# Performance work log

Measured on AMD Instinct MI355X. Metric: run time of the kernel, lower is better.

Reference implementation:

```python
import jax, jax.numpy as jnp
import numpy as np

D_MODEL, D_STATE, D_CONV, EXPAND, N_HEADS = 1024, 64, 4, 2, 8
D_INNER = EXPAND * D_MODEL
D_HEAD = D_INNER // N_HEADS
B, T = 2, 2048
EPS = 1e-6


def setup_inputs() -> dict:
    key = jax.random.key(0)
    ks = jax.random.split(key, 12)
    s = 0.02
    return {
        "x": jax.random.normal(ks[0], (B, T, D_MODEL), jnp.float32),
        "norm_w": jnp.ones((D_MODEL,), jnp.float32),
        "in_w": jax.random.normal(ks[1], (2 * D_INNER, D_MODEL), jnp.float32) * s,
        "conv_w": jax.random.normal(ks[2], (D_INNER, 1, D_CONV), jnp.float32) * s,
        "conv_b": jnp.zeros((D_INNER,), jnp.float32),
        "A_log": jax.random.normal(ks[3], (N_HEADS,), jnp.float32),
        "B_w": jax.random.normal(ks[4], (N_HEADS * D_STATE, D_INNER), jnp.float32) * s,
        "C_w": jax.random.normal(ks[5], (N_HEADS * D_STATE, D_INNER), jnp.float32) * s,
        "dt_w": jax.random.normal(ks[6], (N_HEADS, D_INNER), jnp.float32) * s,
        "dt_b": jnp.zeros((N_HEADS,), jnp.float32),
        "D": jnp.ones((N_HEADS,), jnp.float32),
        "out_w": jax.random.normal(ks[7], (D_MODEL, D_INNER), jnp.float32) * s,
    }


def _rmsnorm(x, w):
    var = jnp.mean(jnp.square(x), axis=-1, keepdims=True)
    return x * jax.lax.rsqrt(var + EPS) * w


def _silu(x):
    return x * jax.nn.sigmoid(x)


def reference(x, norm_w, in_w, conv_w, conv_b, A_log, B_w, C_w, dt_w, dt_b, D, out_w):
    residual = x
    xn = _rmsnorm(x, norm_w)
    xz = xn @ in_w.T                                   # (B,T,2*D_INNER)
    x_ssm, z = jnp.split(xz, 2, axis=-1)

    # causal depthwise conv1d (torch pads both sides by K-1 then slices [:T] == left pad only)
    xc = jnp.transpose(x_ssm, (0, 2, 1))               # (B,C,T)
    xc = jax.lax.conv_general_dilated(
        xc, conv_w, window_strides=(1,), padding=[(D_CONV - 1, 0)],
        feature_group_count=D_INNER,
        dimension_numbers=("NCH", "OIH", "NCH"))
    xc = xc + conv_b[None, :, None]
    x_ssm = _silu(jnp.transpose(xc, (0, 2, 1)))        # (B,T,D_INNER)

    dt = jax.nn.softplus(x_ssm @ dt_w.T + dt_b)        # (B,T,H)
    Bm = (x_ssm @ B_w.T).reshape(B, T, N_HEADS, D_STATE)
    Cm = (x_ssm @ C_w.T).reshape(B, T, N_HEADS, D_STATE)
    xh = x_ssm.reshape(B, T, N_HEADS, D_HEAD)
    A = -jnp.exp(A_log)                                # (H,)

    # time-major for scan
    dt_t = jnp.transpose(dt, (1, 0, 2))                # (T,B,H)
    B_t = jnp.transpose(Bm, (1, 0, 2, 3))              # (T,B,H,N)
    C_t = jnp.transpose(Cm, (1, 0, 2, 3))
    x_t = jnp.transpose(xh, (1, 0, 2, 3))              # (T,B,H,D)

    def step(h, inp):
        dtt, bt, ct, xt = inp
        dA = jnp.exp(dtt * A)[..., None, None]         # (B,H,1,1)
        h = dA * h + dtt[..., None, None] * bt[..., :, None] * xt[..., None, :]
        y = jnp.einsum("bhn,bhnd->bhd", ct, h)
        return h, y

    h0 = jnp.zeros((B, N_HEADS, D_STATE, D_HEAD), x.dtype)
    _, ys = jax.lax.scan(step, h0, (dt_t, B_t, C_t, x_t))  # ys: (T,B,H,D)
    y = jnp.transpose(ys, (1, 0, 2, 3))                # (B,T,H,D)
    y = y + xh * D[None, None, :, None]
    y = y.reshape(B, T, D_INNER)
    y = y * _silu(z)
    out = y @ out_w.T
    return residual + out
```

## Files before the change

kernel.cpp:

```cpp
#include <hip/hip_runtime.h>
#include <hip/hip_bf16.h>
#include <math.h>

#define D_MODEL 1024
#define D_STATE 64
#define D_CONV  4
#define D_INNER 2048
#define N_HEADS 8
#define D_HEAD  256
#define BATCH   2
#define SEQ     2048
#define ROWS    (BATCH*SEQ)
#define NCHUNK  32
#define BCN     1152
#define EPS     1e-6f

typedef __attribute__((ext_vector_type(2))) unsigned short ushort2v;
typedef __attribute__((ext_vector_type(4))) unsigned short ushort4v;
typedef __attribute__((ext_vector_type(8))) unsigned short ushort8v;
typedef __attribute__((ext_vector_type(8))) short short8v;
typedef __attribute__((ext_vector_type(4))) float f32x4;

__device__ __forceinline__ float silu_f(float x){ return x / (1.0f + __expf(-x)); }
__device__ __forceinline__ float softplus_f(float x){ return (x > 20.0f) ? x : log1pf(__expf(x)); }
__device__ __forceinline__ float bf2f(unsigned short u){
    union { unsigned int i; float f; } v; v.i = ((unsigned int)u) << 16; return v.f;
}
__device__ __forceinline__ unsigned short f2bf_bits(float f){
    __hip_bfloat16 h = __float2bfloat16(f);
    return *(unsigned short*)&h;
}
__device__ __forceinline__ void gload_lds16(const void* g, void* l){
    __builtin_amdgcn_global_load_lds((const __attribute__((address_space(1))) void*)g,
                                     (__attribute__((address_space(3))) void*)l, 16, 0, 0);
}
__device__ __forceinline__ void vmw(int n){
    switch(n){
        case 0:  asm volatile("s_waitcnt vmcnt(0)"  ::: "memory"); break;
        case 2:  asm volatile("s_waitcnt vmcnt(2)"  ::: "memory"); break;
        case 3:  asm volatile("s_waitcnt vmcnt(3)"  ::: "memory"); break;
        case 4:  asm volatile("s_waitcnt vmcnt(4)"  ::: "memory"); break;
        case 6:  asm volatile("s_waitcnt vmcnt(6)"  ::: "memory"); break;
        default: asm volatile("s_waitcnt vmcnt(0)"  ::: "memory"); break;
    }
}

__global__ __launch_bounds__(256) void prep_kernel(const float* __restrict__ in_w,
                                                   const float* __restrict__ out_w,
                                                   const float* __restrict__ B_w,
                                                   const float* __restrict__ C_w,
                                                   const float* __restrict__ dt_w,
                                                   unsigned short* __restrict__ inw_bf,
                                                   unsigned short* __restrict__ outw_bf,
                                                   unsigned short* __restrict__ BCw_bf){
    int i = blockIdx.x * 256 + threadIdx.x;
    const float* src; unsigned short* dst; int j;
    if (i < 1048576)      { src = in_w;  dst = inw_bf;            j = i; }
    else if (i < 1572864) { src = out_w; dst = outw_bf;           j = i - 1048576; }
    else if (i < 1835008) { src = B_w;   dst = BCw_bf;            j = i - 1572864; }
    else if (i < 2097152) { src = C_w;   dst = BCw_bf + 1048576;  j = i - 1835008; }
    else {
        int k = i - 2097152;
        int drow = k >> 9;
        int col4 = k & 511;
        ushort4v o = {0,0,0,0};
        if (drow < 8){
            float4 v = ((const float4*)(dt_w + (size_t)drow*D_INNER))[col4];
            o[0] = f2bf_bits(v.x); o[1] = f2bf_bits(v.y);
            o[2] = f2bf_bits(v.z); o[3] = f2bf_bits(v.w);
        }
        ((ushort4v*)(BCw_bf + (size_t)(1024 + drow)*D_INNER))[col4] = o;
        return;
    }
    float4 v = ((const float4*)src)[j];
    ushort4v o;
    o[0] = f2bf_bits(v.x); o[1] = f2bf_bits(v.y);
    o[2] = f2bf_bits(v.z); o[3] = f2bf_bits(v.w);
    ((ushort4v*)dst)[j] = o;
}

__global__ __launch_bounds__(256) void rmsnorm_kernel(const float* __restrict__ x,
                                                      const float* __restrict__ w,
                                                      unsigned short* __restrict__ xn){
    int row = blockIdx.x;
    int tid = threadIdx.x;
    const float4* xr = (const float4*)(x + (size_t)row * D_MODEL);
    float4 a = xr[tid];
    float ss = a.x*a.x + a.y*a.y + a.z*a.z + a.w*a.w;
    #pragma unroll
    for (int i = 1; i < 64; i <<= 1) ss += __shfl_xor(ss, i);
    __shared__ float red[4];
    int lane = tid & 63, wid = tid >> 6;
    if (lane == 0) red[wid] = ss;
    __syncthreads();
    float tot = red[0] + red[1] + red[2] + red[3];
    float scale = rsqrtf(tot * (1.0f / D_MODEL) + EPS);
    float4 wv = ((const float4*)w)[tid];
    ushort4v o;
    o[0] = f2bf_bits(a.x * scale * wv.x);
    o[1] = f2bf_bits(a.y * scale * wv.y);
    o[2] = f2bf_bits(a.z * scale * wv.z);
    o[3] = f2bf_bits(a.w * scale * wv.w);
    ((ushort4v*)(xn + (size_t)row * D_MODEL))[tid] = o;
}

__global__ __launch_bounds__(512) void gemm_in512(const unsigned short* __restrict__ A,
                                                  const unsigned short* __restrict__ W,
                                                  unsigned short* __restrict__ Cout0,
                                                  unsigned short* __restrict__ Cout1){
    const int K = D_MODEL;
    __shared__ unsigned short As[2][256*32];
    __shared__ unsigned short Bs[2][128*32];
    int tid = threadIdx.x;
    int bid = blockIdx.x;
    int x = bid & 7;
    int r = bid >> 3;
    int m0 = ((x & 3)*4 + (r >> 4)) * 256;
    int n0 = ((x >> 2)*16 + (r & 15)) * 128;

    int lane = tid & 63;
    int w = tid >> 6;
    int wrow = w >> 1, wcol = w & 1;
    f32x4 acc[4][4];
    #pragma unroll
    for (int i = 0; i < 4; ++i)
        #pragma unroll
        for (int j = 0; j < 4; ++j) acc[i][j] = (f32x4){0.f,0.f,0.f,0.f};

    int g0 = tid >> 3, s0 = tid & 7;
    int swz0 = (s0*16) ^ ((g0&7)<<4);
    int r0 = 2*g0 + (swz0 >> 6);
    int c0e = (swz0 & 63) >> 1;
    const unsigned short* aS0 = A + (size_t)(m0 + r0)*K + c0e;
    const unsigned short* aS1 = aS0 + (size_t)128*K;
    const unsigned short* bS0 = W + (size_t)(n0 + r0)*K + c0e;

    int frow = lane & 15;
    int fkb  = (lane >> 4) * 16;
    int offA[4], offB[4];
    #pragma unroll
    for (int m = 0; m < 4; ++m){
        int rr = wrow*64 + m*16 + frow;
        int lb = (rr&1)*64 + fkb;
        offA[m] = (rr>>1)*128 + (lb ^ (((rr>>1)&7)<<4));
    }
    #pragma unroll
    for (int n = 0; n < 4; ++n){
        int rr = wcol*64 + n*16 + frow;
        int lb = (rr&1)*64 + fkb;
        offB[n] = (rr>>1)*128 + (lb ^ (((rr>>1)&7)<<4));
    }

    #define STAGE(buf, k0) do{ \
        gload_lds16(aS0 + (k0), &As[buf][(size_t)tid*8]); \
        gload_lds16(aS1 + (k0), &As[buf][(size_t)(tid+512)*8]); \
        gload_lds16(bS0 + (k0), &Bs[buf][(size_t)tid*8]); \
    }while(0)

    #define COMPUTE(buf, tt) do{ \
        short8v af[4], bf[4]; \
        _Pragma("unroll") \
        for (int m = 0; m < 4; ++m) af[m] = *(const short8v*)((const char*)As[buf] + offA[m]); \
        _Pragma("unroll") \
        for (int n = 0; n < 4; ++n) bf[n] = *(const short8v*)((const char*)Bs[buf] + offB[n]); \
        asm volatile("s_waitcnt lgkmcnt(0)" ::: "memory"); \
        __builtin_amdgcn_sched_barrier(0); \
        __builtin_amdgcn_s_barrier(); \
        if ((tt) + 2 < NT) STAGE(buf, (size_t)((tt)+2)*32); \
        _Pragma("unroll") \
        for (int m = 0; m < 4; ++m) \
            _Pragma("unroll") \
            for (int n = 0; n < 4; ++n) \
                acc[m][n] = __builtin_amdgcn_mfma_f32_16x16x32_bf16(af[m], bf[n], acc[m][n], 0, 0, 0); \
    }while(0)

    int NT = K >> 5;
    STAGE(0, 0);
    STAGE(1, 32);
    int t = 0;
    for (; t < NT-1; ++t){
        vmw(3);
        __builtin_amdgcn_sched_barrier(0);
        __builtin_amdgcn_s_barrier();
        COMPUTE(t & 1, t);
    }
    {
        vmw(0);
        __builtin_amdgcn_sched_barrier(0);
        __builtin_amdgcn_s_barrier();
        COMPUTE(t & 1, t);
    }
    #undef COMPUTE
    #undef STAGE

    int rrow = (lane >> 4) * 4;
    int rcol = lane & 15;
    unsigned short* outp;
    int colbase;
    if (n0 < 2048){ outp = Cout0; colbase = n0; }
    else          { outp = Cout1; colbase = n0 - 2048; }
    #pragma unroll
    for (int m = 0; m < 4; ++m)
        #pragma unroll
        for (int n = 0; n < 4; ++n){
            int cc = colbase + wcol*64 + n*16 + rcol;
            #pragma unroll
            for (int i = 0; i < 4; ++i){
                int rr = m0 + wrow*64 + m*16 + rrow + i;
                outp[(size_t)rr*2048 + cc] = f2bf_bits(acc[m][n][i]);
            }
        }
}

template<int MODE, int MAP>
__global__ __launch_bounds__(512) void gemm_k2048(const unsigned short* __restrict__ A,
                                                  const unsigned short* __restrict__ W,
                                                  void* __restrict__ Cout0,
                                                  const float* __restrict__ resid,
                                                  int M, int N, int K){
    __shared__ unsigned short As[4][128*32];
    __shared__ unsigned short Bs[4][128*32];
    int tid = threadIdx.x;
    int bid = blockIdx.x;
    int m0, n0;
    if (MAP == 0){
        int x = bid & 7, sw = bid >> 3;
        int ml = sw >> 2, nl = sw & 3;
        m0 = ((x & 3)*8 + ml) * 128;
        n0 = (((x >> 2)*4) + nl) * 128;
    } else {
        int x = bid & 7, sw = bid >> 3;
        m0 = (x*4 + sw/9) * 128;
        n0 = (sw % 9) * 128;
    }

    int lane = tid & 63;
    int w = tid >> 6;
    int wrow = w >> 2, wcol = w & 3;
    f32x4 acc[4][2];
    #pragma unroll
    for (int i = 0; i < 4; ++i)
        #pragma unroll
        for (int j = 0; j < 2; ++j) acc[i][j] = (f32x4){0.f,0.f,0.f,0.f};

    int g0 = tid >> 3, s0 = tid & 7;
    int swz0 = (s0*16) ^ ((g0&7)<<4);
    int r0 = 2*g0 + (swz0 >> 6);
    int c0e = (swz0 & 63) >> 1;
    const unsigned short* aS = A + (size_t)(m0 + r0)*K + c0e;
    const unsigned short* bS = W + (size_t)(n0 + r0)*K + c0e;

    int frow = lane & 15;
    int fkb  = (lane >> 4) * 16;
    int offA[4], offB[2];
    #pragma unroll
    for (int m = 0; m < 4; ++m){
        int r = wrow*64 + m*16 + frow;
        int lb = (r&1)*64 + fkb;
        offA[m] = (r>>1)*128 + (lb ^ (((r>>1)&7)<<4));
    }
    #pragma unroll
    for (int n = 0; n < 2; ++n){
        int r = wcol*32 + n*16 + frow;
        int lb = (r&1)*64 + fkb;
        offB[n] = (r>>1)*128 + (lb ^ (((r>>1)&7)<<4));
    }

    #define STAGE(buf, k0) do{ \
        gload_lds16(aS + (k0), &As[buf][(size_t)tid*8]); \
        gload_lds16(bS + (k0), &Bs[buf][(size_t)tid*8]); \
    }while(0)

    #define COMPUTE(buf, tt) do{ \
        short8v af[4], bf[2]; \
        _Pragma("unroll") \
        for (int m = 0; m < 4; ++m) af[m] = *(const short8v*)((const char*)As[buf] + offA[m]); \
        _Pragma("unroll") \
        for (int n = 0; n < 2; ++n) bf[n] = *(const short8v*)((const char*)Bs[buf] + offB[n]); \
        asm volatile("s_waitcnt lgkmcnt(0)" ::: "memory"); \
        __builtin_amdgcn_sched_barrier(0); \
        __builtin_amdgcn_s_barrier(); \
        if ((tt) + 4 < NT) STAGE(buf, (size_t)((tt)+4)*32); \
        _Pragma("unroll") \
        for (int m = 0; m < 4; ++m) \
            _Pragma("unroll") \
            for (int n = 0; n < 2; ++n) \
                acc[m][n] = __builtin_amdgcn_mfma_f32_16x16x32_bf16(af[m], bf[n], acc[m][n], 0, 0, 0); \
    }while(0)

    int NT = K >> 5;
    #pragma unroll
    for (int p = 0; p < 4; ++p) STAGE(p, (size_t)p*32);

    int t = 0;
    for (; t < NT-3; ++t){
        vmw(6);
        __builtin_amdgcn_sched_barrier(0);
        __builtin_amdgcn_s_barrier();
        COMPUTE(t & 3, t);
    }
    #pragma unroll
    for (int j = 2; j >= 0; --j){
        vmw(2*j);
        __builtin_amdgcn_sched_barrier(0);
        __builtin_amdgcn_s_barrier();
        COMPUTE(t & 3, t);
        ++t;
    }
    #undef COMPUTE
    #undef STAGE

    int rrow = (lane >> 4) * 4;
    int rcol = lane & 15;
    if (MODE == 2){
        float* Co = (float*)Cout0;
        #pragma unroll
        for (int m = 0; m < 4; ++m)
            #pragma unroll
            for (int n = 0; n < 2; ++n){
                int cc = n0 + wcol*32 + n*16 + rcol;
                #pragma unroll
                for (int i = 0; i < 4; ++i){
                    int rr = m0 + wrow*64 + m*16 + rrow + i;
                    Co[(size_t)rr*N + cc] = acc[m][n][i] + resid[(size_t)rr*N + cc];
                }
            }
    } else {
        unsigned short* outp = (unsigned short*)Cout0;
        #pragma unroll
        for (int m = 0; m < 4; ++m)
            #pragma unroll
            for (int n = 0; n < 2; ++n){
                int cc = n0 + wcol*32 + n*16 + rcol;
                #pragma unroll
                for (int i = 0; i < 4; ++i){
                    int rr = m0 + wrow*64 + m*16 + rrow + i;
                    outp[(size_t)rr*N + cc] = f2bf_bits(acc[m][n][i]);
                }
            }
    }
}

__global__ __launch_bounds__(256) void conv_silu_kernel(const unsigned short* __restrict__ xp,
                                                        const float* __restrict__ cw,
                                                        const float* __restrict__ cb,
                                                        unsigned short* __restrict__ xs){
    int bid = blockIdx.x;
    int r0 = ((bid & 7)*64 + (bid >> 3)) * 8;
    int t0 = r0 & (SEQ - 1);
    int tid = threadIdx.x;
    int c8 = tid*8;

    float4 cwv[8];
    #pragma unroll
    for (int k = 0; k < 8; ++k) cwv[k] = ((const float4*)cw)[c8 + k];
    float cbv[8];
    {
        float4 cb0 = ((const float4*)cb)[tid*2];
        float4 cb1 = ((const float4*)cb)[tid*2+1];
        cbv[0]=cb0.x; cbv[1]=cb0.y; cbv[2]=cb0.z; cbv[3]=cb0.w;
        cbv[4]=cb1.x; cbv[5]=cb1.y; cbv[6]=cb1.z; cbv[7]=cb1.w;
    }

    ushort8v zero8 = {0,0,0,0,0,0,0,0};
    ushort8v xm3, xm2, xm1, cur, nxt;
    if (t0 >= 3){
        xm3 = *(const ushort8v*)(xp + (size_t)(r0-3)*D_INNER + c8);
        xm2 = *(const ushort8v*)(xp + (size_t)(r0-2)*D_INNER + c8);
        xm1 = *(const ushort8v*)(xp + (size_t)(r0-1)*D_INNER + c8);
    } else {
        xm3 = zero8; xm2 = zero8; xm1 = zero8;
    }
    cur = *(const ushort8v*)(xp + (size_t)r0*D_INNER + c8);

    #pragma unroll
    for (int i = 0; i < 8; ++i){
        if (i < 7) nxt = *(const ushort8v*)(xp + (size_t)(r0+i+1)*D_INNER + c8);
        ushort8v o;
        #pragma unroll
        for (int k = 0; k < 8; ++k){
            float a = cbv[k]
                    + bf2f(xm3[k])*cwv[k].x
                    + bf2f(xm2[k])*cwv[k].y
                    + bf2f(xm1[k])*cwv[k].z
                    + bf2f(cur[k])*cwv[k].w;
            o[k] = f2bf_bits(silu_f(a));
        }
        *(ushort8v*)(xs + (size_t)(r0+i)*D_INNER + c8) = o;
        xm3 = xm2; xm2 = xm1; xm1 = cur; cur = nxt;
    }
}

__global__ __launch_bounds__(256) void xdT_kernel(const unsigned short* __restrict__ xs,
                                                  const unsigned short* __restrict__ BCm,
                                                  const float* __restrict__ dt_b,
                                                  const float* __restrict__ A_log,
                                                  unsigned short* __restrict__ xdT,
                                                  float* __restrict__ cums){
    int ct = blockIdx.x, cd = blockIdx.y, bh = blockIdx.z;
    int b = bh >> 3, h = bh & 7;
    __shared__ unsigned short sT[64*68];
    int tid = threadIdx.x;
    float dtbh = dt_b[h];
    if (cd == 0 && tid < 64){
        int t = ct*64 + tid;
        float Ah = -__expf(A_log[h]);
        float raw = bf2f(BCm[(size_t)(b*SEQ + t)*BCN + 1024 + h]);
        float a = softplus_f(raw + dtbh) * Ah;
        #pragma unroll
        for (int i = 1; i < 64; i <<= 1){
            float v = __shfl_up(a, i);
            if (tid >= i) a += v;
        }
        cums[((size_t)bh)*SEQ + t] = a;
    }
    #pragma unroll
    for (int it = 0; it < 2; ++it){
        int l = tid + it*256;
        int tl = l >> 3, seg = l & 7;
        int row = b*SEQ + ct*64 + tl;
        ushort8v v = *(const ushort8v*)(xs + (size_t)row*D_INNER + h*D_HEAD + cd*64 + seg*8);
        float raw = bf2f(BCm[(size_t)row*BCN + 1024 + h]);
        float dtv = softplus_f(raw + dtbh);
        ushort4v lo, hi;
        #pragma unroll
        for (int j = 0; j < 4; ++j){
            lo[j] = f2bf_bits(bf2f(v[j]) * dtv);
            hi[j] = f2bf_bits(bf2f(v[j+4]) * dtv);
        }
        *(ushort4v*)((char*)sT + tl*136 + seg*16)     = lo;
        *(ushort4v*)((char*)sT + tl*136 + seg*16 + 8) = hi;
    }
    __syncthreads();
    #pragma unroll
    for (int it = 0; it < 2; ++it){
        int l = tid + it*256;
        int dl = l >> 3, tseg = l & 7;
        ushort8v o;
        #pragma unroll
        for (int j = 0; j < 8; ++j) o[j] = sT[(tseg*8 + j)*68 + dl];
        *(ushort8v*)(xdT + ((size_t)bh*D_HEAD + cd*64 + dl)*SEQ + ct*64 + tseg*8) = o;
    }
}

__global__ __launch_bounds__(256) void chunk_state_mfma(const unsigned short* __restrict__ xdT,
                                                        const unsigned short* __restrict__ BCm,
                                                        const float* __restrict__ cums,
                                                        unsigned short* __restrict__ HSb){
    int c = blockIdx.x;
    int by = blockIdx.y;
    int h = by >> 1, dh = by & 1;
    int b = blockIdx.z;
    int tid = threadIdx.x;
    int bh = b*N_HEADS + h;
    int t0 = c*64;
    __shared__ unsigned short sX[128*64];
    __shared__ unsigned short sBdT[64*72];
    __shared__ float sdec[64];
    if (tid < 64)
        sdec[tid] = __expf(cums[(size_t)bh*SEQ + t0 + 63] - cums[(size_t)bh*SEQ + t0 + tid]);
    const unsigned short* xb = xdT + ((size_t)bh*D_HEAD + dh*128)*SEQ + t0;
    #pragma unroll
    for (int it = 0; it < 4; ++it){
        int l = tid + it*256;
        int d = l >> 3, seg = l & 7;
        gload_lds16(xb + (size_t)d*SEQ + (((seg*16) ^ ((d&7)<<4)) >> 1),
                    (char*)sX + (size_t)l*16);
    }
    __syncthreads();
    #pragma unroll
    for (int it = 0; it < 2; ++it){
        int l = tid + it*256;
        int tl = l >> 3, seg = l & 7;
        ushort8v bv = *(const ushort8v*)(BCm + (size_t)(b*SEQ + t0 + tl)*BCN + h*64 + seg*8);
        float dec = sdec[tl];
        #pragma unroll
        for (int j = 0; j < 8; ++j)
            sBdT[(seg*8 + j)*72 + tl] = f2bf_bits(bf2f(bv[j]) * dec);
    }
    __syncthreads();

    int lane = tid & 63, w = tid >> 6;
    int d0 = w*32;
    int fr = lane & 15, fk = (lane >> 4)*8;
    f32x4 acc[2][4];
    #pragma unroll
    for (int i = 0; i < 2; ++i)
        #pragma unroll
        for (int j = 0; j < 4; ++j) acc[i][j] = (f32x4){0.f,0.f,0.f,0.f};
    short8v af[2][2], bg[4][2];
    #pragma unroll
    for (int m = 0; m < 2; ++m)
        #pragma unroll
        for (int k = 0; k < 2; ++k){
            int d = d0 + m*16 + fr;
            af[m][k] = *(const short8v*)((const char*)sX + (size_t)d*128 + (((k*32+fk)*2) ^ ((d&7)<<4)));
        }
    #pragma unroll
    for (int n = 0; n < 4; ++n)
        #pragma unroll
        for (int k = 0; k < 2; ++k)
            bg[n][k] = *(const short8v*)(sBdT + (size_t)(n*16 + fr)*72 + k*32 + fk);
    #pragma unroll
    for (int k = 0; k < 2; ++k)
        #pragma unroll
        for (int m = 0; m < 2; ++m)
            #pragma unroll
            for (int n = 0; n < 4; ++n)
                acc[m][n] = __builtin_amdgcn_mfma_f32_16x16x32_bf16(af[m][k], bg[n][k], acc[m][n], 0, 0, 0);

    unsigned short* out = HSb + ((size_t)bh*NCHUNK + c)*16384 + (size_t)dh*128*64;
    int rr = (lane >> 4)*4, rc = lane & 15;
    #pragma unroll
    for (int m = 0; m < 2; ++m)
        #pragma unroll
        for (int n = 0; n < 4; ++n)
            #pragma unroll
            for (int i = 0; i < 4; ++i)
                out[(size_t)(d0 + m*16 + rr + i)*64 + n*16 + rc] = f2bf_bits(acc[m][n][i]);
}

__global__ __launch_bounds__(256) void state_pass_kernel(const float* __restrict__ cums,
                                                         unsigned short* __restrict__ HSb){
    int e2 = blockIdx.x*256 + threadIdx.x;
    int bh = blockIdx.y;
    float Hx = 0.f, Hy = 0.f;
    ushort2v* p = (ushort2v*)(HSb + (size_t)bh*NCHUNK*16384) + e2;
    const float* cp = cums + (size_t)bh*SEQ + 63;
    for (int c = 0; c < NCHUNK; ++c){
        float Pc = __expf(cp[(size_t)c*64]);
        ushort2v s = *p;
        float sx = bf2f(s[0]), sy = bf2f(s[1]);
        ushort2v hold;
        hold[0] = f2bf_bits(Hx); hold[1] = f2bf_bits(Hy);
        *p = hold;
        Hx = fmaf(Pc, Hx, sx);
        Hy = fmaf(Pc, Hy, sy);
        p += 8192;
    }
}

__global__ __launch_bounds__(256) void chunk_out_mfma(const unsigned short* __restrict__ xs,
                                                      const unsigned short* __restrict__ z,
                                                      const unsigned short* __restrict__ BCm,
                                                      const unsigned short* __restrict__ xdT,
                                                      const float* __restrict__ cums,
                                                      const unsigned short* __restrict__ HSb,
                                                      const float* __restrict__ Dp,
                                                      unsigned short* __restrict__ y){
    int c = blockIdx.x;
    int by = blockIdx.y;
    int h = by >> 1, dh = by & 1;
    int b = blockIdx.z;
    int tid = threadIdx.x;
    int bh = b*N_HEADS + h;
    int t0 = c*64;
    __shared__ unsigned short regA[128*64];
    __shared__ unsigned short sW[64*64];
    __shared__ unsigned short sCd[64*64];
    __shared__ float scum[64];
    unsigned short* Craw = regA;
    unsigned short* Braw = regA + 64*64;

    if (tid < 64) scum[tid] = cums[(size_t)bh*SEQ + t0 + tid];
    #pragma unroll
    for (int it = 0; it < 2; ++it){
        int l = tid + it*256;
        int tl = l >> 3, seg = l & 7;
        size_t rowoff = (size_t)(b*SEQ + t0 + tl)*BCN + h*64;
        int soff = ((seg*16) ^ ((tl&7)<<4)) >> 1;
        gload_lds16(BCm + rowoff + 512 + soff, (char*)Craw + (size_t)l*16);
        gload_lds16(BCm + rowoff + soff,       (char*)Braw + (size_t)l*16);
    }
    __syncthreads();

    int lane = tid & 63, w = tid >> 6;
    int fr = lane & 15, fk = (lane >> 4)*8;
    int rr = (lane >> 4)*4, rc = lane & 15;

    int wr = w >> 1, wc = w & 1;
    f32x4 g[2][2];
    #pragma unroll
    for (int i = 0; i < 2; ++i)
        #pragma unroll
        for (int j = 0; j < 2; ++j) g[i][j] = (f32x4){0.f,0.f,0.f,0.f};
    {
        short8v ca[2][2], bb[2][2];
        #pragma unroll
        for (int m = 0; m < 2; ++m)
            #pragma unroll
            for (int k = 0; k < 2; ++k){
                int t = wr*32 + m*16 + fr;
                ca[m][k] = *(const short8v*)((const char*)Craw + (size_t)t*128 + (((k*32+fk)*2) ^ ((t&7)<<4)));
            }
        #pragma unroll
        for (int n = 0; n < 2; ++n)
            #pragma unroll
            for (int k = 0; k < 2; ++k){
                int s = wc*32 + n*16 + fr;
                bb[n][k] = *(const short8v*)((const char*)Braw + (size_t)s*128 + (((k*32+fk)*2) ^ ((s&7)<<4)));
            }
        #pragma unroll
        for (int k = 0; k < 2; ++k)
            #pragma unroll
            for (int m = 0; m < 2; ++m)
                #pragma unroll
                for (int n = 0; n < 2; ++n)
                    g[m][n] = __builtin_amdgcn_mfma_f32_16x16x32_bf16(ca[m][k], bb[n][k], g[m][n], 0, 0, 0);
    }
    #pragma unroll
    for (int m = 0; m < 2; ++m)
        #pragma unroll
        for (int n = 0; n < 2; ++n)
            #pragma unroll
            for (int i = 0; i < 4; ++i){
                int t = wr*32 + m*16 + rr + i;
                int s = wc*32 + n*16 + rc;
                float wv = (s <= t) ? __expf(scum[t] - scum[s]) * g[m][n][i] : 0.f;
                *(unsigned short*)((char*)sW + (size_t)t*128 + ((s*2) ^ ((t&7)<<4))) = f2bf_bits(wv);
            }
    {
        int tl = tid >> 2, sg = tid & 3;
        float ef = __expf(scum[tl]);
        #pragma unroll
        for (int q = 0; q < 2; ++q){
            int off = ((sg*32 + q*16)) ^ ((tl&7)<<4);
            ushort8v cv = *(const ushort8v*)((const char*)Craw + (size_t)tl*128 + off);
            ushort8v ov;
            #pragma unroll
            for (int j = 0; j < 8; ++j) ov[j] = f2bf_bits(bf2f(cv[j]) * ef);
            *(ushort8v*)((char*)sCd + (size_t)tl*128 + off) = ov;
        }
    }
    __syncthreads();

    const unsigned short* xb = xdT + ((size_t)bh*D_HEAD + dh*128)*SEQ + t0;
    #pragma unroll
    for (int it = 0; it < 4; ++it){
        int l = tid + it*256;
        int d = l >> 3, seg = l & 7;
        gload_lds16(xb + (size_t)d*SEQ + (((seg*16) ^ ((d&7)<<4)) >> 1),
                    (char*)regA + (size_t)l*16);
    }
    __syncthreads();

    int d0 = w*32;
    f32x4 acc[4][2];
    #pragma unroll
    for (int i = 0; i < 4; ++i)
        #pragma unroll
        for (int j = 0; j < 2; ++j) acc[i][j] = (f32x4){0.f,0.f,0.f,0.f};
    {
        short8v aw[4][2], xd[2][2];
        #pragma unroll
        for (int m = 0; m < 4; ++m)
            #pragma unroll
            for (int k = 0; k < 2; ++k){
                int t = m*16 + fr;
                aw[m][k] = *(const short8v*)((const char*)sW + (size_t)t*128 + (((k*32+fk)*2) ^ ((t&7)<<4)));
            }
        #pragma unroll
        for (int n = 0; n < 2; ++n)
            #pragma unroll
            for (int k = 0; k < 2; ++k){
                int d = d0 + n*16 + fr;
                xd[n][k] = *(const short8v*)((const char*)regA + (size_t)d*128 + (((k*32+fk)*2) ^ ((d&7)<<4)));
            }
        #pragma unroll
        for (int k = 0; k < 2; ++k)
            #pragma unroll
            for (int m = 0; m < 4; ++m)
                #pragma unroll
                for (int n = 0; n < 2; ++n)
                    acc[m][n] = __builtin_amdgcn_mfma_f32_16x16x32_bf16(aw[m][k], xd[n][k], acc[m][n], 0, 0, 0);
    }
    __syncthreads();

    const unsigned short* hb = HSb + ((size_t)bh*NCHUNK + c)*16384 + (size_t)dh*128*64;
    #pragma unroll
    for (int it = 0; it < 4; ++it){
        int l = tid + it*256;
        int d = l >> 3, seg = l & 7;
        gload_lds16(hb + (size_t)d*64 + (((seg*16) ^ ((d&7)<<4)) >> 1),
                    (char*)regA + (size_t)l*16);
    }
    __syncthreads();

    {
        short8v aw[4][2], ht[2][2];
        #pragma unroll
        for (int m = 0; m < 4; ++m)
            #pragma unroll
            for (int k = 0; k < 2; ++k){
                int t = m*16 + fr;
                aw[m][k] = *(const short8v*)((const char*)sCd + (size_t)t*128 + (((k*32+fk)*2) ^ ((t&7)<<4)));
            }
        #pragma unroll
        for (int n = 0; n < 2; ++n)
            #pragma unroll
            for (int k = 0; k < 2; ++k){
                int d = d0 + n*16 + fr;
                ht[n][k] = *(const short8v*)((const char*)regA + (size_t)d*128 + (((k*32+fk)*2) ^ ((d&7)<<4)));
            }
        #pragma unroll
        for (int k = 0; k < 2; ++k)
            #pragma unroll
            for (int m = 0; m < 4; ++m)
                #pragma unroll
                for (int n = 0; n < 2; ++n)
                    acc[m][n] = __builtin_amdgcn_mfma_f32_16x16x32_bf16(aw[m][k], ht[n][k], acc[m][n], 0, 0, 0);
    }

    float Dh = Dp[h];
    #pragma unroll
    for (int m = 0; m < 4; ++m)
        #pragma unroll
        for (int n = 0; n < 2; ++n)
            #pragma unroll
            for (int i = 0; i < 4; ++i){
                int t = m*16 + rr + i;
                int d = dh*128 + d0 + n*16 + rc;
                size_t off = (size_t)(b*SEQ + t0 + t)*D_INNER + h*D_HEAD + d;
                float val = acc[m][n][i] + Dh * bf2f(xs[off]);
                y[off] = f2bf_bits(val * silu_f(bf2f(z[off])));
            }
}

extern "C" void kernel_launch(void* const* d_in, const int* in_sizes, int n_in,
                              void* d_out, int out_size, void* d_ws, size_t ws_size,
                              hipStream_t stream){
    const float* x      = (const float*)d_in[0];
    const float* norm_w = (const float*)d_in[1];
    const float* in_w   = (const float*)d_in[2];
    const float* conv_w = (const float*)d_in[3];
    const float* conv_b = (const float*)d_in[4];
    const float* A_log  = (const float*)d_in[5];
    const float* B_w    = (const float*)d_in[6];
    const float* C_w    = (const float*)d_in[7];
    const float* dt_w   = (const float*)d_in[8];
    const float* dt_b   = (const float*)d_in[9];
    const float* Dp     = (const float*)d_in[10];
    const float* out_w  = (const float*)d_in[11];
    float* out = (float*)d_out;

    char* ws = (char*)d_ws;
    const size_t MB = 1048576ull;
    unsigned short* xpre_bf = (unsigned short*)(ws);
    unsigned short* y_bf    = xpre_bf;
    unsigned short* z_bf    = (unsigned short*)(ws + 16*MB);
    unsigned short* xs_bf   = (unsigned short*)(ws + 32*MB);
    unsigned short* inw_bf  = (unsigned short*)(ws + 48*MB);
    unsigned short* xdT     = (unsigned short*)(ws + 48*MB);
    unsigned short* HSb     = (unsigned short*)(ws + 64*MB);
    unsigned short* BCm     = (unsigned short*)(ws + 80*MB);
    unsigned short* outw_bf = (unsigned short*)(ws + 90*MB);
    unsigned short* xn_bf   = (unsigned short*)(ws + 94*MB);
    unsigned short* BCw_bf  = (unsigned short*)(ws + 102*MB);
    float*          cums    = (float*)(ws + 107*MB);

    prep_kernel<<<8448, 256, 0, stream>>>(in_w, out_w, B_w, C_w, dt_w,
                                          inw_bf, outw_bf, BCw_bf);

    rmsnorm_kernel<<<ROWS, 256, 0, stream>>>(x, norm_w, xn_bf);

    gemm_in512<<<512, 512, 0, stream>>>(xn_bf, inw_bf, xpre_bf, z_bf);

    conv_silu_kernel<<<512, 256, 0, stream>>>(xpre_bf, conv_w, conv_b, xs_bf);

    gemm_k2048<0,1><<<288, 512, 0, stream>>>(xs_bf, BCw_bf, BCm, nullptr,
        ROWS, BCN, D_INNER);

    xdT_kernel<<<dim3(SEQ/64, D_HEAD/64, BATCH*N_HEADS), 256, 0, stream>>>(xs_bf, BCm, dt_b, A_log, xdT, cums);

    chunk_state_mfma<<<dim3(NCHUNK, N_HEADS*2, BATCH), 256, 0, stream>>>(xdT, BCm, cums, HSb);

    state_pass_kernel<<<dim3(32, BATCH*N_HEADS), 256, 0, stream>>>(cums, HSb);

    chunk_out_mfma<<<dim3(NCHUNK, N_HEADS*2, BATCH), 256, 0, stream>>>(xs_bf, z_bf, BCm, xdT, cums, HSb, Dp, y_bf);

    gemm_k2048<2,0><<<256, 512, 0, stream>>>(y_bf, outw_bf, out, x,
        ROWS, D_MODEL, D_INNER);
}
```

Measured before the change: 172.1 us.

## Fuse rmsnorm into prep, deepen GEMM pipelines, merge xdT column blocks

Folds the RMSNorm into the weight-conversion prep kernel as extra blocks, which removes one launch. The GEMM staging depth becomes a template parameter: 3 buffers for the input projection and 6 for the K=2048 GEMMs, up from 2 and 4, with wait counts adjusted to hide more global-load latency. The xdT kernel now loops over the four column blocks inside one block, computing softplus(dt) once into shared memory rather than per element and per block. The deeper buffers raise LDS use, which may lower occupancy, and the xdT change cuts grid parallelism by four.

```diff
diff --git a/kernel.cpp b/kernel.cpp
--- a/kernel.cpp
+++ b/kernel.cpp
@@ -41,6 +41,8 @@
         case 3:  asm volatile("s_waitcnt vmcnt(3)"  ::: "memory"); break;
         case 4:  asm volatile("s_waitcnt vmcnt(4)"  ::: "memory"); break;
         case 6:  asm volatile("s_waitcnt vmcnt(6)"  ::: "memory"); break;
+        case 8:  asm volatile("s_waitcnt vmcnt(8)"  ::: "memory"); break;
+        case 10: asm volatile("s_waitcnt vmcnt(10)" ::: "memory"); break;
         default: asm volatile("s_waitcnt vmcnt(0)"  ::: "memory"); break;
     }
 }
@@ -50,10 +52,37 @@
                                                    const float* __restrict__ B_w,
                                                    const float* __restrict__ C_w,
                                                    const float* __restrict__ dt_w,
+                                                   const float* __restrict__ x,
+                                                   const float* __restrict__ norm_w,
                                                    unsigned short* __restrict__ inw_bf,
                                                    unsigned short* __restrict__ outw_bf,
-                                                   unsigned short* __restrict__ BCw_bf){
-    int i = blockIdx.x * 256 + threadIdx.x;
+                                                   unsigned short* __restrict__ BCw_bf,
+                                                   unsigned short* __restrict__ xn){
+    __shared__ float red[4];
+    int bid = blockIdx.x;
+    int tid = threadIdx.x;
+    if (bid >= 8448){
+        int row = bid - 8448;
+        const float4* xr = (const float4*)(x + (size_t)row * D_MODEL);
+        float4 a = xr[tid];
+        float ss = a.x*a.x + a.y*a.y + a.z*a.z + a.w*a.w;
+        #pragma unroll
+        for (int i = 1; i < 64; i <<= 1) ss += __shfl_xor(ss, i);
+        int lane = tid & 63, wid = tid >> 6;
+        if (lane == 0) red[wid] = ss;
+        __syncthreads();
+        float tot = red[0] + red[1] + red[2] + red[3];
+        float scale = rsqrtf(tot * (1.0f / D_MODEL) + EPS);
+        float4 wv = ((const float4*)norm_w)[tid];
+        ushort4v o;
+        o[0] = f2bf_bits(a.x * scale * wv.x);
+        o[1] = f2bf_bits(a.y * scale * wv.y);
+        o[2] = f2bf_bits(a.z * scale * wv.z);
+        o[3] = f2bf_bits(a.w * scale * wv.w);
+        ((ushort4v*)(xn + (size_t)row * D_MODEL))[tid] = o;
+        return;
+    }
+    int i = bid * 256 + tid;
     const float* src; unsigned short* dst; int j;
     if (i < 1048576)      { src = in_w;  dst = inw_bf;            j = i; }
     else if (i < 1572864) { src = out_w; dst = outw_bf;           j = i - 1048576; }
@@ -79,38 +108,14 @@
     ((ushort4v*)dst)[j] = o;
 }
 
-__global__ __launch_bounds__(256) void rmsnorm_kernel(const float* __restrict__ x,
-                                                      const float* __restrict__ w,
-                                                      unsigned short* __restrict__ xn){
-    int row = blockIdx.x;
-    int tid = threadIdx.x;
-    const float4* xr = (const float4*)(x + (size_t)row * D_MODEL);
-    float4 a = xr[tid];
-    float ss = a.x*a.x + a.y*a.y + a.z*a.z + a.w*a.w;
-    #pragma unroll
-    for (int i = 1; i < 64; i <<= 1) ss += __shfl_xor(ss, i);
-    __shared__ float red[4];
-    int lane = tid & 63, wid = tid >> 6;
-    if (lane == 0) red[wid] = ss;
-    __syncthreads();
-    float tot = red[0] + red[1] + red[2] + red[3];
-    float scale = rsqrtf(tot * (1.0f / D_MODEL) + EPS);
-    float4 wv = ((const float4*)w)[tid];
-    ushort4v o;
-    o[0] = f2bf_bits(a.x * scale * wv.x);
-    o[1] = f2bf_bits(a.y * scale * wv.y);
-    o[2] = f2bf_bits(a.z * scale * wv.z);
-    o[3] = f2bf_bits(a.w * scale * wv.w);
-    ((ushort4v*)(xn + (size_t)row * D_MODEL))[tid] = o;
-}
-
+template<int DEPTH>
 __global__ __launch_bounds__(512) void gemm_in512(const unsigned short* __restrict__ A,
                                                   const unsigned short* __restrict__ W,
                                                   unsigned short* __restrict__ Cout0,
                                                   unsigned short* __restrict__ Cout1){
     const int K = D_MODEL;
-    __shared__ unsigned short As[2][256*32];
-    __shared__ unsigned short Bs[2][128*32];
+    __shared__ unsigned short As[DEPTH][256*32];
+    __shared__ unsigned short Bs[DEPTH][128*32];
     int tid = threadIdx.x;
     int bid = blockIdx.x;
     int x = bid & 7;
@@ -166,7 +171,7 @@
         asm volatile("s_waitcnt lgkmcnt(0)" ::: "memory"); \
         __builtin_amdgcn_sched_barrier(0); \
         __builtin_amdgcn_s_barrier(); \
-        if ((tt) + 2 < NT) STAGE(buf, (size_t)((tt)+2)*32); \
+        if ((tt) + DEPTH < NT) STAGE(buf, (size_t)((tt)+DEPTH)*32); \
         _Pragma("unroll") \
         for (int m = 0; m < 4; ++m) \
             _Pragma("unroll") \
@@ -175,20 +180,25 @@
     }while(0)
 
     int NT = K >> 5;
-    STAGE(0, 0);
-    STAGE(1, 32);
-    int t = 0;
-    for (; t < NT-1; ++t){
-        vmw(3);
+    #pragma unroll
+    for (int p = 0; p < DEPTH; ++p) STAGE(p, (size_t)p*32);
+
+    int t = 0, cur = 0;
+    for (; t < NT-(DEPTH-1); ++t){
+        vmw(3*(DEPTH-1));
         __builtin_amdgcn_sched_barrier(0);
         __builtin_amdgcn_s_barrier();
-        COMPUTE(t & 1, t);
-    }
-    {
-        vmw(0);
+        COMPUTE(cur, t);
+        cur = (cur+1 == DEPTH) ? 0 : cur+1;
+    }
+    #pragma unroll
+    for (int j = DEPTH-2; j >= 0; --j){
+        vmw(3*j);
         __builtin_amdgcn_sched_barrier(0);
         __builtin_amdgcn_s_barrier();
-        COMPUTE(t & 1, t);
+        COMPUTE(cur, t);
+        ++t;
+        cur = (cur+1 == DEPTH) ? 0 : cur+1;
     }
     #undef COMPUTE
     #undef STAGE
@@ -212,14 +222,14 @@
         }
 }
 
-template<int MODE, int MAP>
+template<int MODE, int MAP, int DEPTH>
 __global__ __launch_bounds__(512) void gemm_k2048(const unsigned short* __restrict__ A,
                                                   const unsigned short* __restrict__ W,
                                                   void* __restrict__ Cout0,
                                                   const float* __restrict__ resid,
                                                   int M, int N, int K){
-    __shared__ unsigned short As[4][128*32];
-    __shared__ unsigned short Bs[4][128*32];
+    __shared__ unsigned short As[DEPTH][128*32];
+    __shared__ unsigned short Bs[DEPTH][128*32];
     int tid = threadIdx.x;
     int bid = blockIdx.x;
     int m0, n0;
@@ -280,7 +290,7 @@
         asm volatile("s_waitcnt lgkmcnt(0)" ::: "memory"); \
         __builtin_amdgcn_sched_barrier(0); \
         __builtin_amdgcn_s_barrier(); \
-        if ((tt) + 4 < NT) STAGE(buf, (size_t)((tt)+4)*32); \
+        if ((tt) + DEPTH < NT) STAGE(buf, (size_t)((tt)+DEPTH)*32); \
         _Pragma("unroll") \
         for (int m = 0; m < 4; ++m) \
             _Pragma("unroll") \
@@ -290,22 +300,24 @@
 
     int NT = K >> 5;
     #pragma unroll
-    for (int p = 0; p < 4; ++p) STAGE(p, (size_t)p*32);
-
-    int t = 0;
-    for (; t < NT-3; ++t){
-        vmw(6);
+    for (int p = 0; p < DEPTH; ++p) STAGE(p, (size_t)p*32);
+
+    int t = 0, cur = 0;
+    for (; t < NT-(DEPTH-1); ++t){
+        vmw(2*(DEPTH-1));
         __builtin_amdgcn_sched_barrier(0);
         __builtin_amdgcn_s_barrier();
-        COMPUTE(t & 3, t);
-    }
-    #pragma unroll
-    for (int j = 2; j >= 0; --j){
+        COMPUTE(cur, t);
+        cur = (cur+1 == DEPTH) ? 0 : cur+1;
+    }
+    #pragma unroll
+    for (int j = DEPTH-2; j >= 0; --j){
         vmw(2*j);
         __builtin_amdgcn_sched_barrier(0);
         __builtin_amdgcn_s_barrier();
-        COMPUTE(t & 3, t);
+        COMPUTE(cur, t);
         ++t;
+        cur = (cur+1 == DEPTH) ? 0 : cur+1;
     }
     #undef COMPUTE
     #undef STAGE
@@ -397,16 +409,18 @@
                                                   const float* __restrict__ A_log,
                                                   unsigned short* __restrict__ xdT,
                                                   float* __restrict__ cums){
-    int ct = blockIdx.x, cd = blockIdx.y, bh = blockIdx.z;
+    int ct = blockIdx.x, bh = blockIdx.y;
     int b = bh >> 3, h = bh & 7;
     __shared__ unsigned short sT[64*68];
+    __shared__ float sdt[64];
     int tid = threadIdx.x;
-    float dtbh = dt_b[h];
-    if (cd == 0 && tid < 64){
+    if (tid < 64){
         int t = ct*64 + tid;
+        float raw = bf2f(BCm[(size_t)(b*SEQ + t)*BCN + 1024 + h]);
+        float dtv = softplus_f(raw + dt_b[h]);
+        sdt[tid] = dtv;
         float Ah = -__expf(A_log[h]);
-        float raw = bf2f(BCm[(size_t)(b*SEQ + t)*BCN + 1024 + h]);
-        float a = softplus_f(raw + dtbh) * Ah;
+        float a = dtv * Ah;
         #pragma unroll
         for (int i = 1; i < 64; i <<= 1){
             float v = __shfl_up(a, i);
@@ -414,32 +428,35 @@
         }
         cums[((size_t)bh)*SEQ + t] = a;
     }
-    #pragma unroll
-    for (int it = 0; it < 2; ++it){
-        int l = tid + it*256;
-        int tl = l >> 3, seg = l & 7;
-        int row = b*SEQ + ct*64 + tl;
-        ushort8v v = *(const ushort8v*)(xs + (size_t)row*D_INNER + h*D_HEAD + cd*64 + seg*8);
-        float raw = bf2f(BCm[(size_t)row*BCN + 1024 + h]);
-        float dtv = softplus_f(raw + dtbh);
-        ushort4v lo, hi;
-        #pragma unroll
-        for (int j = 0; j < 4; ++j){
-            lo[j] = f2bf_bits(bf2f(v[j]) * dtv);
-            hi[j] = f2bf_bits(bf2f(v[j+4]) * dtv);
+    __syncthreads();
+    for (int cd = 0; cd < 4; ++cd){
+        #pragma unroll
+        for (int it = 0; it < 2; ++it){
+            int l = tid + it*256;
+            int tl = l >> 3, seg = l & 7;
+            int row = b*SEQ + ct*64 + tl;
+            ushort8v v = *(const ushort8v*)(xs + (size_t)row*D_INNER + h*D_HEAD + cd*64 + seg*8);
+            float dtv = sdt[tl];
+            ushort4v lo, hi;
+            #pragma unroll
+            for (int j = 0; j < 4; ++j){
+                lo[j] = f2bf_bits(bf2f(v[j]) * dtv);
+                hi[j] = f2bf_bits(bf2f(v[j+4]) * dtv);
+            }
+            *(ushort4v*)((char*)sT + tl*136 + seg*16)     = lo;
+            *(ushort4v*)((char*)sT + tl*136 + seg*16 + 8) = hi;
         }
-        *(ushort4v*)((char*)sT + tl*136 + seg*16)     = lo;
-        *(ushort4v*)((char*)sT + tl*136 + seg*16 + 8) = hi;
-    }
-    __syncthreads();
-    #pragma unroll
-    for (int it = 0; it < 2; ++it){
-        int l = tid + it*256;
-        int dl = l >> 3, tseg = l & 7;
-        ushort8v o;
-        #pragma unroll
-        for (int j = 0; j < 8; ++j) o[j] = sT[(tseg*8 + j)*68 + dl];
-        *(ushort8v*)(xdT + ((size_t)bh*D_HEAD + cd*64 + dl)*SEQ + ct*64 + tseg*8) = o;
+        __syncthreads();
+        #pragma unroll
+        for (int it = 0; it < 2; ++it){
+            int l = tid + it*256;
+            int dl = l >> 3, tseg = l & 7;
+            ushort8v o;
+            #pragma unroll
+            for (int j = 0; j < 8; ++j) o[j] = sT[(tseg*8 + j)*68 + dl];
+            *(ushort8v*)(xdT + ((size_t)bh*D_HEAD + cd*64 + dl)*SEQ + ct*64 + tseg*8) = o;
+        }
+        __syncthreads();
     }
 }
 
@@ -758,19 +775,17 @@
     unsigned short* BCw_bf  = (unsigned short*)(ws + 102*MB);
     float*          cums    = (float*)(ws + 107*MB);
 
-    prep_kernel<<<8448, 256, 0, stream>>>(in_w, out_w, B_w, C_w, dt_w,
-                                          inw_bf, outw_bf, BCw_bf);
-
-    rmsnorm_kernel<<<ROWS, 256, 0, stream>>>(x, norm_w, xn_bf);
-
-    gemm_in512<<<512, 512, 0, stream>>>(xn_bf, inw_bf, xpre_bf, z_bf);
+    prep_kernel<<<12544, 256, 0, stream>>>(in_w, out_w, B_w, C_w, dt_w, x, norm_w,
+                                           inw_bf, outw_bf, BCw_bf, xn_bf);
+
+    gemm_in512<3><<<512, 512, 0, stream>>>(xn_bf, inw_bf, xpre_bf, z_bf);
 
     conv_silu_kernel<<<512, 256, 0, stream>>>(xpre_bf, conv_w, conv_b, xs_bf);
 
-    gemm_k2048<0,1><<<288, 512, 0, stream>>>(xs_bf, BCw_bf, BCm, nullptr,
+    gemm_k2048<0,1,6><<<288, 512, 0, stream>>>(xs_bf, BCw_bf, BCm, nullptr,
         ROWS, BCN, D_INNER);
 
-    xdT_kernel<<<dim3(SEQ/64, D_HEAD/64, BATCH*N_HEADS), 256, 0, stream>>>(xs_bf, BCm, dt_b, A_log, xdT, cums);
+    xdT_kernel<<<dim3(SEQ/64, BATCH*N_HEADS), 256, 0, stream>>>(xs_bf, BCm, dt_b, A_log, xdT, cums);
 
     chunk_state_mfma<<<dim3(NCHUNK, N_HEADS*2, BATCH), 256, 0, stream>>>(xdT, BCm, cums, HSb);
 
@@ -778,6 +793,6 @@
 
     chunk_out_mfma<<<dim3(NCHUNK, N_HEADS*2, BATCH), 256, 0, stream>>>(xs_bf, z_bf, BCm, xdT, cums, HSb, Dp, y_bf);
 
-    gemm_k2048<2,0><<<256, 512, 0, stream>>>(y_bf, outw_bf, out, x,
+    gemm_k2048<2,0,6><<<256, 512, 0, stream>>>(y_bf, outw_bf, out, x,
         ROWS, D_MODEL, D_INNER);
 }
```

After: 195.7 us. +13.7%, slower.
